# Kernel optimization log

Measured on AMD Instinct MI355X. Metric: run time of the kernel, lower is better.

## Reference

```python
import jax, jax.numpy as jnp
import numpy as np

S, B, D, H, OUT = 512, 200, 64, 256, 3  # B == window_len - 2 = 200
EPS = 1e-5


def setup_inputs() -> dict:
    key = jax.random.key(0)
    ks = jax.random.split(key, 16)
    f = lambda k, sh, s=0.05: jax.random.normal(k, sh, dtype=jnp.float32) * s
    return {
        "x": f(ks[0], (S, B, D), 1.0),
        "w_ih0": f(ks[1], (3 * H, D)), "w_hh0": f(ks[2], (3 * H, H)),
        "b_ih0": f(ks[3], (3 * H,)), "b_hh0": f(ks[4], (3 * H,)),
        "w_ih1": f(ks[5], (3 * H, H)), "w_hh1": f(ks[6], (3 * H, H)),
        "b_ih1": f(ks[7], (3 * H,)), "b_hh1": f(ks[8], (3 * H,)),
        "ln_w": jnp.ones((H,), jnp.float32), "ln_b": jnp.zeros((H,), jnp.float32),
        "fc2_w": f(ks[9], (512, B * H), 0.01), "fc2_b": f(ks[10], (512,)),
        "bn_g": jnp.ones((512,), jnp.float32), "bn_b": jnp.zeros((512,), jnp.float32),
        "fc3_w": f(ks[11], (OUT, 512)), "fc3_b": f(ks[12], (OUT,)),
    }


def _gru_layer(x, w_ih, w_hh, b_ih, b_hh):
    # x: (S, B, D_in) -> (S, B, H), torch nn.GRU gate order [r, z, n]
    gi = jnp.einsum('sbd,gd->sbg', x, w_ih) + b_ih  # precompute input gates
    h0 = jnp.zeros((x.shape[1], w_hh.shape[1]), x.dtype)

    def step(h, gi_t):
        gh = h @ w_hh.T + b_hh
        ir, iz, inn = jnp.split(gi_t, 3, axis=-1)
        hr, hz, hn = jnp.split(gh, 3, axis=-1)
        r = jax.nn.sigmoid(ir + hr)
        z = jax.nn.sigmoid(iz + hz)
        n = jnp.tanh(inn + r * hn)
        h_new = (1.0 - z) * n + z * h
        return h_new, h_new

    _, hs = jax.lax.scan(step, h0, gi)
    return hs


def reference(x, w_ih0, w_hh0, b_ih0, b_hh0, w_ih1, w_hh1, b_ih1, b_hh1,
              ln_w, ln_b, fc2_w, fc2_b, bn_g, bn_b, fc3_w, fc3_b):
    h = _gru_layer(x, w_ih0, w_hh0, b_ih0, b_hh0)
    h = _gru_layer(h, w_ih1, w_hh1, b_ih1, b_hh1)
    # LayerNorm over hidden dim, then ReLU
    mu = jnp.mean(h, axis=-1, keepdims=True)
    var = jnp.var(h, axis=-1, keepdims=True)
    h = (h - mu) * jax.lax.rsqrt(var + EPS) * ln_w + ln_b
    h = jax.nn.relu(h)
    # flatten: (S, B*H)
    h = h.reshape(h.shape[0], -1)
    y = h @ fc2_w.T + fc2_b
    # BatchNorm1d (training mode: batch stats over axis 0, biased var)
    mu2 = jnp.mean(y, axis=0)
    var2 = jnp.var(y, axis=0)
    y = (y - mu2) * jax.lax.rsqrt(var2 + EPS) * bn_g + bn_b
    y = jax.nn.relu(y)
    return y @ fc3_w.T + fc3_b
```

## Files before the change

### kernel.cpp

```cpp
#include <hip/hip_runtime.h>
#include <stdint.h>

typedef _Float16 f16;
typedef _Float16 f16x4 __attribute__((ext_vector_type(4)));
typedef _Float16 f16x8 __attribute__((ext_vector_type(8)));
typedef float f32x4 __attribute__((ext_vector_type(4)));

#define SEQ 512
#define NB  200
#define HD  256
#define GD  768
#define BW  16
#define NBLK 13
#define GI_TSTRIDE (NBLK*12288)
#define LOG2E 1.44269504f

__device__ __forceinline__ f32x4 mfma16(f16x8 a, f16x8 b, f32x4 c){
  return __builtin_amdgcn_mfma_f32_16x16x32_f16(a, b, c, 0, 0, 0);
}

__global__ void cvt_f32_f16(const float* __restrict__ src, f16* __restrict__ dst, int n4){
  int i = blockIdx.x * blockDim.x + threadIdx.x;
  int stride = gridDim.x * blockDim.x;
  for (; i < n4; i += stride){
    float4 v = ((const float4*)src)[i];
    f16x4 o = { (f16)v.x, (f16)v.y, (f16)v.z, (f16)v.w };
    ((f16x4*)dst)[i] = o;
  }
}

template<int MODE>
__global__ __launch_bounds__(256, 2)
void gemm_bt(const f16* __restrict__ A, const f16* __restrict__ B,
             f16* __restrict__ Cb, float* __restrict__ Cf,
             const float* __restrict__ bias1, const float* __restrict__ bias2,
             int K, int N, int klen)
{
  const int l  = threadIdx.x & 63;
  const int w  = threadIdx.x >> 6;
  const int lr = l & 15, lg = l >> 4;
  const int Mb = blockIdx.x * 128 + (w >> 1) * 64;
  const int Nb = blockIdx.y * 128 + (w & 1) * 64;
  const int kb = blockIdx.z * klen;

  const f16* Ap = A + (size_t)(Mb + lr) * K + kb + lg * 8;
  const f16* Bp = B + (size_t)(Nb + lr) * K + kb + lg * 8;

  f32x4 acc[4][4];
  #pragma unroll
  for (int i = 0; i < 4; ++i)
    #pragma unroll
    for (int j = 0; j < 4; ++j)
      acc[i][j] = (f32x4){0.f, 0.f, 0.f, 0.f};

  for (int k = 0; k < klen; k += 32){
    f16x8 af[4], bfr[4];
    #pragma unroll
    for (int i = 0; i < 4; ++i){
      af[i]  = *(const f16x8*)(Ap + (size_t)i * 16 * K + k);
      bfr[i] = *(const f16x8*)(Bp + (size_t)i * 16 * K + k);
    }
    #pragma unroll
    for (int i = 0; i < 4; ++i)
      #pragma unroll
      for (int j = 0; j < 4; ++j)
        acc[i][j] = mfma16(af[i], bfr[j], acc[i][j]);
  }

  if (MODE == 0){
    float bv[4];
    #pragma unroll
    for (int j = 0; j < 4; ++j){
      int g = Nb + j*16 + lr;
      bv[j] = bias1[g] + (g < 512 ? bias2[g] : 0.f);
    }
    #pragma unroll
    for (int i = 0; i < 4; ++i)
      #pragma unroll
      for (int r = 0; r < 4; ++r){
        int row = Mb + i*16 + lg*4 + r;
        int t = (int)(((uint64_t)(uint32_t)row * 167773u) >> 25);
        int b = row - t*200;
        int bblk = b >> 4, blr = b & 15;
        size_t region = ((size_t)t*NBLK + bblk) * 12288;
        #pragma unroll
        for (int j = 0; j < 4; ++j){
          int g = Nb + j*16 + lr;
          int q = g >> 8, jj = g & 255;
          int ww = jj >> 4, jr = jj & 15;
          int lane = (jr >> 2)*16 + blr;
          size_t idx;
          if (q < 2) idx = region + (size_t)ww*512 + lane*8 + q*4 + (jr & 3);
          else       idx = region + (size_t)(16 + (ww>>1))*512 + (ww&1)*256 + lane*4 + (jr & 3);
          Cb[idx] = (f16)(acc[i][j][r] + bv[j]);
        }
      }
  } else {
    #pragma unroll
    for (int i = 0; i < 4; ++i)
      #pragma unroll
      for (int j = 0; j < 4; ++j)
        #pragma unroll
        for (int r = 0; r < 4; ++r){
          int row = Mb + i*16 + lg*4 + r;
          int col = Nb + j*16 + lr;
          Cf[((size_t)blockIdx.z * 512 + row) * N + col] = acc[i][j][r];
        }
  }
}

__global__
__attribute__((amdgpu_flat_work_group_size(1024, 1024), amdgpu_waves_per_eu(4, 4)))
void gru_layer(const f16* __restrict__ whh, const float* __restrict__ bhh,
               const f16* __restrict__ gi, f16* __restrict__ hs)
{
  __shared__ __align__(16) unsigned char sm[16384 + 49152 + 32768];
  const int tid = threadIdx.x;
  const int w  = tid >> 6, l = tid & 63;
  const int lr = l & 15, lg = l >> 4;
  const int b0 = blockIdx.x * BW;
  const bool bval = (b0 + lr) < NB;

  ((int2*)sm)[tid] = make_int2(0,0);

  const int nchunk = 16 + (w >> 1);
  const f16* glane = gi + (size_t)blockIdx.x * 12288 + l*8;
#define DMA_GI(P) do { \
    __builtin_amdgcn_global_load_lds( \
        (const __attribute__((address_space(1))) void*)(glane + w*512), \
        (__attribute__((address_space(3))) void*)(sm + 16384 + (P)*24576 + w*1024), \
        16, 0, 0); \
    __builtin_amdgcn_global_load_lds( \
        (const __attribute__((address_space(1))) void*)(glane + nchunk*512), \
        (__attribute__((address_space(3))) void*)(sm + 16384 + (P)*24576 + nchunk*1024), \
        16, 0, 0); \
  } while(0)

  DMA_GI(0);

  f16x8 wA[3][8];
  #pragma unroll
  for (int q = 0; q < 3; ++q)
    #pragma unroll
    for (int kk = 0; kk < 8; ++kk)
      wA[q][kk] = *(const f16x8*)(whh + (size_t)(q*256 + w*16 + lr)*256 + kk*32 + lg*8);

  #pragma unroll
  for (int q = 0; q < 3; ++q)
    #pragma unroll
    for (int kk = 0; kk < 8; ++kk)
      asm volatile("" : "+v"(wA[q][kk]));

  f16x4 bnv;
  {
    float4 bv = *(const float4*)(bhh + 512 + w*16 + lg*4);
    bnv = (f16x4){(f16)bv.x,(f16)bv.y,(f16)bv.z,(f16)bv.w};
  }

  const int cswz = ((lr ^ (lr >> 2)) & 3) << 4;
  const int hrd  = lr*64 + ((lg*16) ^ cswz);
  const int girz = 16384 + w*1024 + l*16;
  const int gin  = 16384 + nchunk*1024 + (w&1)*512 + l*8;
  const int hwb  = (w>>1)*1024 + lr*64 + ((((w&1)*32) + lg*8) ^ cswz);

  f16* hp = hs + (size_t)(b0 + lr)*HD + w*16 + lg*4;
  f16x4 hvp = (f16x4){(f16)0.f,(f16)0.f,(f16)0.f,(f16)0.f};

  asm volatile("s_waitcnt vmcnt(0)" ::: "memory");
  __syncthreads();

#define GRUSTEP(P) do { \
    asm volatile("s_waitcnt vmcnt(0)" ::: "memory");  \
    f32x4 a0 = {0.f,0.f,0.f,0.f}, a1 = {0.f,0.f,0.f,0.f}; \
    f32x4 a2 = {(float)bnv[0],(float)bnv[1],(float)bnv[2],(float)bnv[3]}; \
    glane += GI_TSTRIDE; \
    DMA_GI((P)^1); \
    _Pragma("unroll") \
    for (int kk = 0; kk < 8; ++kk){ \
      f16x8 hf = *(const f16x8*)(sm + (P)*8192 + kk*1024 + hrd); \
      a0 = mfma16(wA[0][kk], hf, a0); \
      a1 = mfma16(wA[1][kk], hf, a1); \
      a2 = mfma16(wA[2][kk], hf, a2); \
    } \
    f16x8 rz = *(const f16x8*)(sm + (P)*24576 + girz); \
    f16x4 nn = *(const f16x4*)(sm + (P)*24576 + gin); \
    f16x4 hv; \
    _Pragma("unroll") \
    for (int r = 0; r < 4; ++r){ \
      float rg = __builtin_amdgcn_rcpf(1.f + __builtin_amdgcn_exp2f(-LOG2E*((float)rz[r] + a0[r]))); \
      float zg = __builtin_amdgcn_rcpf(1.f + __builtin_amdgcn_exp2f(-LOG2E*((float)rz[4+r] + a1[r]))); \
      float aa = (float)nn[r] + rg*a2[r]; \
      float ng = 2.f*__builtin_amdgcn_rcpf(1.f + __builtin_amdgcn_exp2f(-2.f*LOG2E*aa)) - 1.f; \
      float h  = ng + zg*((float)hvp[r] - ng); \
      hv[r] = (f16)h; \
    } \
    hvp = hv; \
    *(f16x4*)(sm + ((P)^1)*8192 + hwb) = hv; \
    if (bval) *(f16x4*)hp = hv; \
    hp += (size_t)NB*HD; \
    asm volatile("s_waitcnt lgkmcnt(0)" ::: "memory"); \
    __builtin_amdgcn_sched_barrier(0); \
    __builtin_amdgcn_s_barrier(); \
    __builtin_amdgcn_sched_barrier(0); \
  } while(0)

  for (int th = 0; th < SEQ/2; ++th){
    GRUSTEP(0);
    GRUSTEP(1);
  }
#undef GRUSTEP
#undef DMA_GI
}

__global__ __launch_bounds__(256)
void ln_relu(f16* __restrict__ hs, const float* __restrict__ lnw,
             const float* __restrict__ lnb)
{
  const int tid = threadIdx.x;
  const int wv = tid >> 6;
  const int lane = tid & 63;
  const int half = lane >> 5;
  const int c0 = (lane & 31) * 8;
  float gw[8], gb[8];
  #pragma unroll
  for (int r = 0; r < 8; ++r){ gw[r] = lnw[c0 + r]; gb[r] = lnb[c0 + r]; }
  const int npairs = SEQ * NB / 2;
  for (int pair = blockIdx.x * 4 + wv; pair < npairs; pair += gridDim.x * 4){
    f16* p = hs + (size_t)(pair*2 + half) * HD + c0;
    f16x8 v = *(const f16x8*)p;
    float f[8], s = 0.f, q = 0.f;
    #pragma unroll
    for (int r = 0; r < 8; ++r){ f[r] = (float)v[r]; s += f[r]; q += f[r]*f[r]; }
    #pragma unroll
    for (int off = 16; off; off >>= 1){
      s += __shfl_xor(s, off);
      q += __shfl_xor(q, off);
    }
    float mu = s * (1.f / HD);
    float var = q * (1.f / HD) - mu * mu;
    float rs = rsqrtf(var + 1e-5f);
    f16x8 o;
    #pragma unroll
    for (int r = 0; r < 8; ++r){
      float y = (f[r] - mu) * rs * gw[r] + gb[r];
      o[r] = (f16)fmaxf(y, 0.f);
    }
    *(f16x8*)p = o;
  }
}

__global__ __launch_bounds__(512)
void bn_relu(const float* __restrict__ part, const float* __restrict__ g,
             const float* __restrict__ b, float* __restrict__ z)
{
  __shared__ float lds[16];
  const int o = blockIdx.x, s = threadIdx.x, w = s >> 6;
  float y = 0.f;
  #pragma unroll
  for (int p = 0; p < 8; ++p) y += part[((size_t)p * 512 + o) * 512 + s];
  float su = y, q = y * y;
  #pragma unroll
  for (int off = 32; off; off >>= 1){
    su += __shfl_down(su, off);
    q  += __shfl_down(q, off);
  }
  if ((s & 63) == 0){ lds[w] = su; lds[8 + w] = q; }
  __syncthreads();
  float S = 0.f, Q = 0.f;
  #pragma unroll
  for (int i = 0; i < 8; ++i){ S += lds[i]; Q += lds[8 + i]; }
  float mu = S * (1.f / 512.f);
  float var = Q * (1.f / 512.f) - mu * mu;
  float zz = fmaxf((y - mu) * rsqrtf(var + 1e-5f) * g[o] + b[o], 0.f);
  z[(size_t)o * 512 + s] = zz;
}

__global__ __launch_bounds__(256)
void fc3_k(const float* __restrict__ z, const float* __restrict__ w,
           const float* __restrict__ b, float* __restrict__ out)
{
  __shared__ float lds[12];
  const int s = blockIdx.x, tid = threadIdx.x, wv = tid >> 6;
  float a0 = 0.f, a1 = 0.f, a2 = 0.f;
  for (int o = tid; o < 512; o += 256){
    float zz = z[(size_t)o * 512 + s];
    a0 += zz * w[o];
    a1 += zz * w[512 + o];
    a2 += zz * w[1024 + o];
  }
  #pragma unroll
  for (int off = 32; off; off >>= 1){
    a0 += __shfl_down(a0, off);
    a1 += __shfl_down(a1, off);
    a2 += __shfl_down(a2, off);
  }
  if ((tid & 63) == 0){ lds[wv] = a0; lds[4 + wv] = a1; lds[8 + wv] = a2; }
  __syncthreads();
  if (tid == 0){
    out[s*3 + 0] = lds[0] + lds[1] + lds[2]  + lds[3]  + b[0];
    out[s*3 + 1] = lds[4] + lds[5] + lds[6]  + lds[7]  + b[1];
    out[s*3 + 2] = lds[8] + lds[9] + lds[10] + lds[11] + b[2];
  }
}

extern "C" void kernel_launch(void* const* d_in, const int* in_sizes, int n_in,
                              void* d_out, int out_size, void* d_ws, size_t ws_size,
                              hipStream_t stream)
{
  (void)in_sizes; (void)n_in; (void)out_size; (void)ws_size;
  const float* x    = (const float*)d_in[0];
  const float* wih0 = (const float*)d_in[1];
  const float* whh0 = (const float*)d_in[2];
  const float* bih0 = (const float*)d_in[3];
  const float* bhh0 = (const float*)d_in[4];
  const float* wih1 = (const float*)d_in[5];
  const float* whh1 = (const float*)d_in[6];
  const float* bih1 = (const float*)d_in[7];
  const float* bhh1 = (const float*)d_in[8];
  const float* lnw  = (const float*)d_in[9];
  const float* lnb  = (const float*)d_in[10];
  const float* fc2w = (const float*)d_in[11];
  const float* bng  = (const float*)d_in[13];
  const float* bnb  = (const float*)d_in[14];
  const float* fc3w = (const float*)d_in[15];
  const float* fc3b = (const float*)d_in[16];
  float* out = (float*)d_out;

  char* ws = (char*)d_ws;
  size_t off = 0;
  auto alloc = [&](size_t bytes) -> void* {
    void* p = ws + off; off += (bytes + 255) & ~(size_t)255; return p;
  };
  f16* GI     = (f16*)alloc((size_t)SEQ*GI_TSTRIDE*2);
  f16* X16    = (f16*)alloc((size_t)SEQ*NB*64*2);
  f16* WI0    = (f16*)alloc((size_t)768*64*2);
  f16* WH0    = (f16*)alloc((size_t)768*256*2);
  f16* WI1    = (f16*)alloc((size_t)768*256*2);
  f16* WH1    = (f16*)alloc((size_t)768*256*2);
  f16* HS0    = (f16*)alloc((size_t)SEQ*NB*256*2);
  f16* HS1    = (f16*)alloc((size_t)SEQ*NB*256*2);
  float* PART = (float*)alloc((size_t)8*512*512*4);
  float* Z    = (float*)alloc((size_t)512*512*4);
  f16* FC2W   = GI;

  cvt_f32_f16<<<2048,256,0,stream>>>(x,    X16,  SEQ*NB*64/4);
  cvt_f32_f16<<<64,  256,0,stream>>>(wih0, WI0,  768*64/4);
  cvt_f32_f16<<<192, 256,0,stream>>>(whh0, WH0,  768*256/4);
  cvt_f32_f16<<<192, 256,0,stream>>>(wih1, WI1,  768*256/4);
  cvt_f32_f16<<<192, 256,0,stream>>>(whh1, WH1,  768*256/4);

  dim3 g0(800, 6, 1);
  gemm_bt<0><<<g0, 256, 0, stream>>>(X16, WI0, GI, nullptr, bih0, bhh0, 64, GD, 64);
  gru_layer<<<NBLK, 1024, 0, stream>>>(WH0, bhh0, GI, HS0);
  gemm_bt<0><<<g0, 256, 0, stream>>>(HS0, WI1, GI, nullptr, bih1, bhh1, 256, GD, 256);
  gru_layer<<<NBLK, 1024, 0, stream>>>(WH1, bhh1, GI, HS1);
  ln_relu<<<3200, 256, 0, stream>>>(HS1, lnw, lnb);
  cvt_f32_f16<<<4096,256,0,stream>>>(fc2w, FC2W, 512*51200/4);
  dim3 g2(4, 4, 8);
  gemm_bt<1><<<g2, 256, 0, stream>>>(FC2W, HS1, nullptr, PART, nullptr, nullptr, 51200, 512, 6400);
  bn_relu<<<512, 512, 0, stream>>>(PART, bng, bnb, Z);
  fc3_k<<<512, 256, 0, stream>>>(Z, fc3w, fc3b, out);
}
```

Baseline: 3.147 ms.

## Shrink GRU block to four waves with split register/LDS/global W_hh storage

The recurrent GRU kernel now runs 256 threads per block instead of 1024, so each wave computes 64 hidden units (12 MFMA tiles) rather than 16. W_hh is split three ways: three tiles stay in registers, three are staged in LDS, and six are re-read from global memory (hopefully L2/L1-resident) every step. The input-gate GEMM epilogue layout and the DMA of input gates are rewritten to match the new per-wave ownership. The aim is to cut the per-step barrier cost across 16 waves and raise MFMA density per wave, at the risk of per-step global weight reloads and serialized MFMA latency on fewer waves.

```diff
diff --git a/kernel.cpp b/kernel.cpp
--- a/kernel.cpp
+++ b/kernel.cpp
@@ -14,6 +14,8 @@
 #define NBLK 13
 #define GI_TSTRIDE (NBLK*12288)
 #define LOG2E 1.44269504f
+#define SMH 98304
+#define SMG 114688
 
 __device__ __forceinline__ f32x4 mfma16(f16x8 a, f16x8 b, f32x4 c){
   return __builtin_amdgcn_mfma_f32_16x16x32_f16(a, b, c, 0, 0, 0);
@@ -86,12 +88,13 @@
         #pragma unroll
         for (int j = 0; j < 4; ++j){
           int g = Nb + j*16 + lr;
-          int q = g >> 8, jj = g & 255;
-          int ww = jj >> 4, jr = jj & 15;
-          int lane = (jr >> 2)*16 + blr;
+          int q = g >> 8, jp = g & 255;
+          int ww = jp >> 6, jj = jp & 63;
+          int t4 = jj >> 4, lg2 = (jj >> 2) & 3, rr = jj & 3;
+          int lane = lg2*16 + blr;
           size_t idx;
-          if (q < 2) idx = region + (size_t)ww*512 + lane*8 + q*4 + (jr & 3);
-          else       idx = region + (size_t)(16 + (ww>>1))*512 + (ww&1)*256 + lane*4 + (jr & 3);
+          if (q < 2) idx = region + (size_t)(ww*6 + t4)*512 + lane*8 + q*4 + rr;
+          else       idx = region + (size_t)(ww*6 + 4 + (t4>>1))*512 + lane*8 + (t4&1)*4 + rr;
           Cb[idx] = (f16)(acc[i][j][r] + bv[j]);
         }
       }
@@ -110,93 +113,134 @@
 }
 
 __global__
-__attribute__((amdgpu_flat_work_group_size(1024, 1024), amdgpu_waves_per_eu(4, 4)))
+__attribute__((amdgpu_flat_work_group_size(256, 256), amdgpu_waves_per_eu(1, 1)))
 void gru_layer(const f16* __restrict__ whh, const float* __restrict__ bhh,
                const f16* __restrict__ gi, f16* __restrict__ hs)
 {
-  __shared__ __align__(16) unsigned char sm[16384 + 49152 + 32768];
+  __shared__ __align__(16) unsigned char sm[163840];
   const int tid = threadIdx.x;
   const int w  = tid >> 6, l = tid & 63;
   const int lr = l & 15, lg = l >> 4;
   const int b0 = blockIdx.x * BW;
   const bool bval = (b0 + lr) < NB;
 
-  ((int2*)sm)[tid] = make_int2(0,0);
-
-  const int nchunk = 16 + (w >> 1);
-  const f16* glane = gi + (size_t)blockIdx.x * 12288 + l*8;
+  ((int4*)(sm + SMH))[tid]       = make_int4(0,0,0,0);
+  ((int4*)(sm + SMH))[tid + 256] = make_int4(0,0,0,0);
+
+  const f16* glane = gi + (size_t)blockIdx.x*12288 + w*3072 + l*8;
 #define DMA_GI(P) do { \
-    __builtin_amdgcn_global_load_lds( \
-        (const __attribute__((address_space(1))) void*)(glane + w*512), \
-        (__attribute__((address_space(3))) void*)(sm + 16384 + (P)*24576 + w*1024), \
-        16, 0, 0); \
-    __builtin_amdgcn_global_load_lds( \
-        (const __attribute__((address_space(1))) void*)(glane + nchunk*512), \
-        (__attribute__((address_space(3))) void*)(sm + 16384 + (P)*24576 + nchunk*1024), \
-        16, 0, 0); \
+    _Pragma("unroll") \
+    for (int c = 0; c < 6; ++c) \
+      __builtin_amdgcn_global_load_lds( \
+          (const __attribute__((address_space(1))) void*)(glane + c*512), \
+          (__attribute__((address_space(3))) void*)(sm + SMG + (P)*24576 + w*6144 + c*1024), \
+          16, 0, 0); \
   } while(0)
 
   DMA_GI(0);
 
-  f16x8 wA[3][8];
-  #pragma unroll
-  for (int q = 0; q < 3; ++q)
+  {
+    const int SQ[3] = {0,1,1}, ST[3] = {3,0,1};
+    #pragma unroll
+    for (int s = 0; s < 3; ++s)
+      #pragma unroll
+      for (int kk = 0; kk < 8; ++kk){
+        f16x8 v = *(const f16x8*)(whh + (size_t)(SQ[s]*256 + w*64 + ST[s]*16 + lr)*256 + kk*32 + lg*8);
+        *(f16x8*)(sm + w*24576 + s*8192 + kk*1024 + l*16) = v;
+      }
+  }
+
+  f16x8 wR[3][8];
+  #pragma unroll
+  for (int t = 0; t < 3; ++t)
     #pragma unroll
     for (int kk = 0; kk < 8; ++kk)
-      wA[q][kk] = *(const f16x8*)(whh + (size_t)(q*256 + w*16 + lr)*256 + kk*32 + lg*8);
-
-  #pragma unroll
-  for (int q = 0; q < 3; ++q)
+      wR[t][kk] = *(const f16x8*)(whh + (size_t)(w*64 + t*16 + lr)*256 + kk*32 + lg*8);
+  #pragma unroll
+  for (int t = 0; t < 3; ++t)
     #pragma unroll
     for (int kk = 0; kk < 8; ++kk)
-      asm volatile("" : "+v"(wA[q][kk]));
-
-  f16x4 bnv;
-  {
-    float4 bv = *(const float4*)(bhh + 512 + w*16 + lg*4);
-    bnv = (f16x4){(f16)bv.x,(f16)bv.y,(f16)bv.z,(f16)bv.w};
+      asm volatile("" : "+v"(wR[t][kk]));
+
+  const int MQ[6] = {1,1,2,2,2,2}, MT[6] = {2,3,0,1,2,3};
+  const f16* wS[6];
+  #pragma unroll
+  for (int m = 0; m < 6; ++m)
+    wS[m] = whh + (size_t)(MQ[m]*256 + w*64 + MT[m]*16 + lr)*256 + lg*8;
+
+  f32x4 bn4[4];
+  #pragma unroll
+  for (int t4 = 0; t4 < 4; ++t4){
+    float4 bv = *(const float4*)(bhh + 512 + w*64 + t4*16 + lg*4);
+    bn4[t4] = (f32x4){bv.x, bv.y, bv.z, bv.w};
   }
 
   const int cswz = ((lr ^ (lr >> 2)) & 3) << 4;
-  const int hrd  = lr*64 + ((lg*16) ^ cswz);
-  const int girz = 16384 + w*1024 + l*16;
-  const int gin  = 16384 + nchunk*1024 + (w&1)*512 + l*8;
-  const int hwb  = (w>>1)*1024 + lr*64 + ((((w&1)*32) + lg*8) ^ cswz);
-
-  f16* hp = hs + (size_t)(b0 + lr)*HD + w*16 + lg*4;
-  f16x4 hvp = (f16x4){(f16)0.f,(f16)0.f,(f16)0.f,(f16)0.f};
+  const int hrd = SMH + lr*64 + ((lg*16) ^ cswz);
+  const int gib = SMG + w*6144 + l*16;
+
+  f16* hp = hs + (size_t)(b0 + lr)*HD + w*64 + lg*4;
+  f16x4 hv0p = (f16x4){(f16)0.f,(f16)0.f,(f16)0.f,(f16)0.f};
+  f16x4 hv1p = hv0p, hv2p = hv0p, hv3p = hv0p;
 
   asm volatile("s_waitcnt vmcnt(0)" ::: "memory");
   __syncthreads();
 
+#define GATE(P, T4, AR, AZ, AN, HVP) do { \
+    f16x8 rz = *(const f16x8*)(sm + (P)*24576 + gib + (T4)*1024); \
+    f16x4 nn = *(const f16x4*)(sm + (P)*24576 + gib + (4+((T4)>>1))*1024 + ((T4)&1)*8); \
+    f16x4 hv; \
+    _Pragma("unroll") \
+    for (int r = 0; r < 4; ++r){ \
+      float rg = __builtin_amdgcn_rcpf(1.f + __builtin_amdgcn_exp2f(-LOG2E*((float)rz[r] + AR[r]))); \
+      float zg = __builtin_amdgcn_rcpf(1.f + __builtin_amdgcn_exp2f(-LOG2E*((float)rz[4+r] + AZ[r]))); \
+      float aa = (float)nn[r] + rg*AN[r]; \
+      float ng = 2.f*__builtin_amdgcn_rcpf(1.f + __builtin_amdgcn_exp2f(-2.f*LOG2E*aa)) - 1.f; \
+      float h  = ng + zg*((float)HVP[r] - ng); \
+      hv[r] = (f16)h; \
+    } \
+    HVP = hv; \
+    *(f16x4*)(sm + SMH + ((P)^1)*8192 + (w*2 + ((T4)>>1))*1024 + lr*64 \
+              + ((((T4)&1)*32 | (lg*8)) ^ cswz)) = hv; \
+    if (bval) *(f16x4*)(hp + (T4)*16) = hv; \
+  } while(0)
+
 #define GRUSTEP(P) do { \
     asm volatile("s_waitcnt vmcnt(0)" ::: "memory");  \
-    f32x4 a0 = {0.f,0.f,0.f,0.f}, a1 = {0.f,0.f,0.f,0.f}; \
-    f32x4 a2 = {(float)bnv[0],(float)bnv[1],(float)bnv[2],(float)bnv[3]}; \
+    f32x4 aR0={0.f,0.f,0.f,0.f}, aR1=aR0, aR2=aR0, aR3=aR0; \
+    f32x4 aZ0=aR0, aZ1=aR0, aZ2=aR0, aZ3=aR0; \
+    f32x4 aN0=bn4[0], aN1=bn4[1], aN2=bn4[2], aN3=bn4[3]; \
     glane += GI_TSTRIDE; \
     DMA_GI((P)^1); \
     _Pragma("unroll") \
     for (int kk = 0; kk < 8; ++kk){ \
       f16x8 hf = *(const f16x8*)(sm + (P)*8192 + kk*1024 + hrd); \
-      a0 = mfma16(wA[0][kk], hf, a0); \
-      a1 = mfma16(wA[1][kk], hf, a1); \
-      a2 = mfma16(wA[2][kk], hf, a2); \
+      aR0 = mfma16(wR[0][kk], hf, aR0); \
+      aR1 = mfma16(wR[1][kk], hf, aR1); \
+      aR2 = mfma16(wR[2][kk], hf, aR2); \
+      f16x8 l0 = *(const f16x8*)(sm + w*24576 + 0*8192 + kk*1024 + l*16); \
+      f16x8 l1 = *(const f16x8*)(sm + w*24576 + 1*8192 + kk*1024 + l*16); \
+      f16x8 l2 = *(const f16x8*)(sm + w*24576 + 2*8192 + kk*1024 + l*16); \
+      aR3 = mfma16(l0, hf, aR3); \
+      aZ0 = mfma16(l1, hf, aZ0); \
+      aZ1 = mfma16(l2, hf, aZ1); \
+      f16x8 s0 = *(const f16x8*)(wS[0] + kk*32); \
+      f16x8 s1 = *(const f16x8*)(wS[1] + kk*32); \
+      f16x8 s2 = *(const f16x8*)(wS[2] + kk*32); \
+      f16x8 s3 = *(const f16x8*)(wS[3] + kk*32); \
+      f16x8 s4 = *(const f16x8*)(wS[4] + kk*32); \
+      f16x8 s5 = *(const f16x8*)(wS[5] + kk*32); \
+      aZ2 = mfma16(s0, hf, aZ2); \
+      aZ3 = mfma16(s1, hf, aZ3); \
+      aN0 = mfma16(s2, hf, aN0); \
+      aN1 = mfma16(s3, hf, aN1); \
+      aN2 = mfma16(s4, hf, aN2); \
+      aN3 = mfma16(s5, hf, aN3); \
     } \
-    f16x8 rz = *(const f16x8*)(sm + (P)*24576 + girz); \
-    f16x4 nn = *(const f16x4*)(sm + (P)*24576 + gin); \
-    f16x4 hv; \
-    _Pragma("unroll") \
-    for (int r = 0; r < 4; ++r){ \
-      float rg = __builtin_amdgcn_rcpf(1.f + __builtin_amdgcn_exp2f(-LOG2E*((float)rz[r] + a0[r]))); \
-      float zg = __builtin_amdgcn_rcpf(1.f + __builtin_amdgcn_exp2f(-LOG2E*((float)rz[4+r] + a1[r]))); \
-      float aa = (float)nn[r] + rg*a2[r]; \
-      float ng = 2.f*__builtin_amdgcn_rcpf(1.f + __builtin_amdgcn_exp2f(-2.f*LOG2E*aa)) - 1.f; \
-      float h  = ng + zg*((float)hvp[r] - ng); \
-      hv[r] = (f16)h; \
-    } \
-    hvp = hv; \
-    *(f16x4*)(sm + ((P)^1)*8192 + hwb) = hv; \
-    if (bval) *(f16x4*)hp = hv; \
+    GATE(P, 0, aR0, aZ0, aN0, hv0p); \
+    GATE(P, 1, aR1, aZ1, aN1, hv1p); \
+    GATE(P, 2, aR2, aZ2, aN2, hv2p); \
+    GATE(P, 3, aR3, aZ3, aN3, hv3p); \
     hp += (size_t)NB*HD; \
     asm volatile("s_waitcnt lgkmcnt(0)" ::: "memory"); \
     __builtin_amdgcn_sched_barrier(0); \
@@ -209,6 +253,7 @@
     GRUSTEP(1);
   }
 #undef GRUSTEP
+#undef GATE
 #undef DMA_GI
 }
 
@@ -351,9 +396,9 @@
 
   dim3 g0(800, 6, 1);
   gemm_bt<0><<<g0, 256, 0, stream>>>(X16, WI0, GI, nullptr, bih0, bhh0, 64, GD, 64);
-  gru_layer<<<NBLK, 1024, 0, stream>>>(WH0, bhh0, GI, HS0);
+  gru_layer<<<NBLK, 256, 0, stream>>>(WH0, bhh0, GI, HS0);
   gemm_bt<0><<<g0, 256, 0, stream>>>(HS0, WI1, GI, nullptr, bih1, bhh1, 256, GD, 256);
-  gru_layer<<<NBLK, 1024, 0, stream>>>(WH1, bhh1, GI, HS1);
+  gru_layer<<<NBLK, 256, 0, stream>>>(WH1, bhh1, GI, HS1);
   ln_relu<<<3200, 256, 0, stream>>>(HS1, lnw, lnb);
   cvt_f32_f16<<<4096,256,0,stream>>>(fc2w, FC2W, 512*51200/4);
   dim3 g2(4, 4, 8);
```

Measured after the change: 7.379 ms. 134% more time.
